# Kernel tuning notes

Hardware: AMD Instinct MI355X
Metric: run time of the kernel (lower is better)

Reference implementation:

```python
import jax, jax.numpy as jnp
import numpy as np

N_NODES = 50000


def setup_inputs() -> dict:
    key = jax.random.key(0)
    ks = jax.random.split(key, 5)
    d_in, d_out = 512, 512
    n_edges = 800000
    x = jax.random.normal(ks[0], (N_NODES, d_in), dtype=jnp.float32)
    edge_index = jax.random.randint(ks[1], (2, n_edges), 0, N_NODES, dtype=jnp.int64)
    s = 1.0 / np.sqrt(d_in)
    W_l = jax.random.uniform(ks[2], (d_out, d_in), dtype=jnp.float32, minval=-s, maxval=s)
    b_l = jax.random.uniform(ks[3], (d_out,), dtype=jnp.float32, minval=-s, maxval=s)
    W_r = jax.random.uniform(ks[4], (d_out, d_in), dtype=jnp.float32, minval=-s, maxval=s)
    return {"x": x, "edge_index": edge_index, "W_l": W_l, "b_l": b_l, "W_r": W_r}


def reference(x, edge_index, W_l, b_l, W_r):
    # lin_l: dense transform before aggregation
    x_l = x @ W_l.T + b_l                       # [N, d_out]
    src, dst = edge_index[0], edge_index[1]
    # sparse adjacency matmul (SAGE mean-neighbor aggregation):
    # out_l[i] = mean_{j in N(i)} x_l[j]
    agg = jax.ops.segment_sum(x_l[src], dst, num_segments=N_NODES)   # [N, d_out]
    deg = jax.ops.segment_sum(jnp.ones_like(src, dtype=x.dtype), dst,
                              num_segments=N_NODES)                  # [N]
    out_l = agg / jnp.maximum(deg, 1.0)[:, None]
    # lin_r: self-loop transform (no bias)
    out_r = x @ W_r.T
    return out_l + out_r
```

## Files before the change

kernel.cpp:

```cpp
#include <hip/hip_runtime.h>

typedef __bf16 bf16x8 __attribute__((ext_vector_type(8)));
typedef float floatx4 __attribute__((ext_vector_type(4)));
typedef float floatx2 __attribute__((ext_vector_type(2)));
typedef unsigned short ushortx8 __attribute__((ext_vector_type(8)));

__device__ __forceinline__ unsigned short f2b(float f) {
    union { float f; unsigned u; } v; v.f = f;
    unsigned r = v.u + 0x7fffu + ((v.u >> 16) & 1u);
    return (unsigned short)(r >> 16);
}


__global__ void deg_count_kernel(const int* __restrict__ dst, int* __restrict__ deg, int nE) {
    int e = blockIdx.x * blockDim.x + threadIdx.x;
    if (e < nE) atomicAdd(&deg[dst[e]], 1);
}

__global__ void scan1_kernel(const int* __restrict__ deg, int* __restrict__ bsum, int n) {
    __shared__ int s[256];
    int b = blockIdx.x, t = threadIdx.x;
    int base = b * 1024 + t * 4;
    int v = 0;
#pragma unroll
    for (int i = 0; i < 4; i++) { int idx = base + i; if (idx < n) v += deg[idx]; }
    s[t] = v; __syncthreads();
    for (int o = 128; o > 0; o >>= 1) { if (t < o) s[t] += s[t + o]; __syncthreads(); }
    if (t == 0) bsum[b] = s[0];
}

__global__ void scan2_kernel(int* __restrict__ bsum, int* __restrict__ off, int nb, int n) {
    if (threadIdx.x == 0) {
        int acc = 0;
        for (int i = 0; i < nb; i++) { int x = bsum[i]; bsum[i] = acc; acc += x; }
        off[n] = acc;
    }
}

__global__ void scan3_kernel(const int* __restrict__ deg, const int* __restrict__ bsum,
                             int* __restrict__ off, int n) {
    __shared__ int s[256];
    int b = blockIdx.x, t = threadIdx.x;
    int idx = b * 1024 + t * 4;
    int a0 = (idx     < n) ? deg[idx]     : 0;
    int a1 = (idx + 1 < n) ? deg[idx + 1] : 0;
    int a2 = (idx + 2 < n) ? deg[idx + 2] : 0;
    int a3 = (idx + 3 < n) ? deg[idx + 3] : 0;
    int tsum = a0 + a1 + a2 + a3;
    s[t] = tsum; __syncthreads();
    for (int o = 1; o < 256; o <<= 1) {
        int u = (t >= o) ? s[t - o] : 0;
        __syncthreads();
        s[t] += u;
        __syncthreads();
    }
    int excl = s[t] - tsum + bsum[b];
    if (idx     < n) off[idx]     = excl;
    if (idx + 1 < n) off[idx + 1] = excl + a0;
    if (idx + 2 < n) off[idx + 2] = excl + a0 + a1;
    if (idx + 3 < n) off[idx + 3] = excl + a0 + a1 + a2;
}

__global__ void fill_kernel(const int* __restrict__ src, const int* __restrict__ dst,
                            const int* __restrict__ off, int* __restrict__ cursor,
                            int* __restrict__ csr, int nE) {
    int e = blockIdx.x * blockDim.x + threadIdx.x;
    if (e < nE) {
        int d = dst[e];
        int pos = atomicAdd(&cursor[d], 1);
        csr[off[d] + pos] = src[e];
    }
}


__global__ void convx_kernel(const float* __restrict__ x, unsigned short* __restrict__ Abuf,
                             unsigned char* __restrict__ X8, int Mreal, int Mpad) {
    long t = (long)blockIdx.x * blockDim.x + threadIdx.x;
    long row = t >> 6;
    int c8 = (int)(t & 63) * 8;
    if (row >= Mpad) return;
    if (row < Mreal) {
        const float4* p4 = (const float4*)(x + row * 512 + c8);
        float4 v0 = p4[0], v1 = p4[1];
        ushortx8 o8;
        o8[0] = f2b(v0.x); o8[1] = f2b(v0.y); o8[2] = f2b(v0.z); o8[3] = f2b(v0.w);
        o8[4] = f2b(v1.x); o8[5] = f2b(v1.y); o8[6] = f2b(v1.z); o8[7] = f2b(v1.w);
        *(ushortx8*)(Abuf + row * 1024 + 512 + c8) = o8;
        unsigned int pa = __builtin_amdgcn_cvt_pk_fp8_f32(v0.x, v0.y, 0, false);
        pa = __builtin_amdgcn_cvt_pk_fp8_f32(v0.z, v0.w, pa, true);
        unsigned int pb = __builtin_amdgcn_cvt_pk_fp8_f32(v1.x, v1.y, 0, false);
        pb = __builtin_amdgcn_cvt_pk_fp8_f32(v1.z, v1.w, pb, true);
        *(uint2*)(X8 + row * 512 + c8) = make_uint2(pa, pb);
    } else {
        ushortx8 z = {0, 0, 0, 0, 0, 0, 0, 0};
        *(ushortx8*)(Abuf + row * 1024 + c8) = z;
        *(ushortx8*)(Abuf + row * 1024 + 512 + c8) = z;
    }
}


__global__ void agg_kernel(const unsigned char* __restrict__ X8,
                           const int* __restrict__ off, const int* __restrict__ csr,
                           unsigned short* __restrict__ Abuf_w, int n) {
    int wid = (int)((blockIdx.x * (long)blockDim.x + threadIdx.x) >> 6);
    int l = threadIdx.x & 63;
    if (wid >= n) return;
    int beg = off[wid], end = off[wid + 1];
    float a[8] = {};
    int e = beg;
    while (e < end) {
        int cnt = end - e; if (cnt > 64) cnt = 64;
        int myi = csr[e + (l < cnt ? l : cnt - 1)];
        for (int j = 0; j < cnt; j++) {
            int s = __builtin_amdgcn_readlane(myi, j);
            uint2 p = *(const uint2*)(X8 + (long)s * 512 + l * 8);
            floatx2 f0 = __builtin_amdgcn_cvt_pk_f32_fp8(p.x, false);
            floatx2 f1 = __builtin_amdgcn_cvt_pk_f32_fp8(p.x, true);
            floatx2 f2 = __builtin_amdgcn_cvt_pk_f32_fp8(p.y, false);
            floatx2 f3 = __builtin_amdgcn_cvt_pk_f32_fp8(p.y, true);
            a[0] += f0[0]; a[1] += f0[1]; a[2] += f1[0]; a[3] += f1[1];
            a[4] += f2[0]; a[5] += f2[1]; a[6] += f3[0]; a[7] += f3[1];
        }
        e += cnt;
    }
    int d = end - beg;
    float inv = 1.0f / (float)(d > 0 ? d : 1);
    ushortx8 o8;
#pragma unroll
    for (int i = 0; i < 8; i++) o8[i] = f2b(a[i] * inv);
    *(ushortx8*)(Abuf_w + (long)wid * 1024 + l * 8) = o8;
}


__global__ void convw_kernel(const float* __restrict__ Wl, const float* __restrict__ Wr,
                             unsigned short* __restrict__ Wcat) {
    int t = blockIdx.x * blockDim.x + threadIdx.x;
    int o = t >> 7;
    int c8 = (t & 127) * 8;
    const float* p = (c8 < 512) ? (Wl + o * 512 + c8) : (Wr + o * 512 + (c8 - 512));
    float4 v0 = ((const float4*)p)[0], v1 = ((const float4*)p)[1];
    ushortx8 o8;
    o8[0] = f2b(v0.x); o8[1] = f2b(v0.y); o8[2] = f2b(v0.z); o8[3] = f2b(v0.w);
    o8[4] = f2b(v1.x); o8[5] = f2b(v1.y); o8[6] = f2b(v1.z); o8[7] = f2b(v1.w);
    *(ushortx8*)(Wcat + (long)o * 1024 + c8) = o8;
}


__global__ __launch_bounds__(256, 2)
void gemm_kernel(const unsigned short* __restrict__ A, const unsigned short* __restrict__ B,
                 const float* __restrict__ bl, const int* __restrict__ deg,
                 float* __restrict__ out, int Mreal) {
    __shared__ unsigned short As[128 * 32];
    __shared__ unsigned short Bs[128 * 32];
    int tid = threadIdx.x;
    int w = tid >> 6, l = tid & 63;
    long i0 = (long)blockIdx.y * 128;
    int n0 = blockIdx.x * 128;
    int wm = (w >> 1) * 64, wn = (w & 1) * 64;
    int r = l & 15, q = l >> 4;
    int srow = l >> 2;
    int sch = (l & 3) * 8;

    floatx4 acc[4][4] = {};

    for (int k0 = 0; k0 < 1024; k0 += 32) {
#pragma unroll
        for (int j = 0; j < 2; j++) {
            int s = w * 2 + j;
            int row = s * 16 + srow;
            const unsigned short* ga = A + (i0 + row) * 1024 + k0 + sch;
            const unsigned short* gb = B + (long)(n0 + row) * 1024 + k0 + sch;
            __builtin_amdgcn_global_load_lds(
                (__attribute__((address_space(1))) void*)(uintptr_t)ga,
                (__attribute__((address_space(3))) void*)(uintptr_t)(As + s * 512), 16, 0, 0);
            __builtin_amdgcn_global_load_lds(
                (__attribute__((address_space(1))) void*)(uintptr_t)gb,
                (__attribute__((address_space(3))) void*)(uintptr_t)(Bs + s * 512), 16, 0, 0);
        }
        __syncthreads();
        bf16x8 af[4], bfr[4];
#pragma unroll
        for (int a = 0; a < 4; a++)
            af[a] = *(const bf16x8*)(As + (wm + a * 16 + r) * 32 + q * 8);
#pragma unroll
        for (int b = 0; b < 4; b++)
            bfr[b] = *(const bf16x8*)(Bs + (wn + b * 16 + r) * 32 + q * 8);
#pragma unroll
        for (int a = 0; a < 4; a++)
#pragma unroll
            for (int b = 0; b < 4; b++)
                acc[a][b] = __builtin_amdgcn_mfma_f32_16x16x32_bf16(af[a], bfr[b], acc[a][b], 0, 0, 0);
        __syncthreads();
    }

#pragma unroll
    for (int a = 0; a < 4; a++) {
        long rb = i0 + wm + a * 16 + q * 4;
#pragma unroll
        for (int rr = 0; rr < 4; rr++) {
            long row = rb + rr;
            if (row < Mreal) {
                bool hasdeg = deg[row] > 0;
#pragma unroll
                for (int b = 0; b < 4; b++) {
                    int col = n0 + wn + b * 16 + r;
                    float v = acc[a][b][rr];
                    if (hasdeg) v += bl[col];
                    out[row * 512 + col] = v;
                }
            }
        }
    }
}


extern "C" void kernel_launch(void* const* d_in, const int* in_sizes, int n_in,
                              void* d_out, int out_size, void* d_ws, size_t ws_size,
                              hipStream_t stream) {
    const float* x  = (const float*)d_in[0];
    const int* eidx = (const int*)d_in[1];
    const float* Wl = (const float*)d_in[2];
    const float* bl = (const float*)d_in[3];
    const float* Wr = (const float*)d_in[4];
    float* out = (float*)d_out;

    int N  = in_sizes[0] / 512;
    int nE = in_sizes[1] / 2;
    const int* src = eidx;
    const int* dst = eidx + nE;
    int Mpad = (N + 127) & ~127;
    int nb = (N + 1023) / 1024;

    char* w = (char*)d_ws;
    size_t o = 0;
    auto alloc = [&](size_t bytes) { void* p = w + o; o = (o + bytes + 255) & ~255UL; return p; };
    int* deg    = (int*)alloc((size_t)N * 4);
    int* cursor = (int*)alloc((size_t)N * 4);
    int* off    = (int*)alloc((size_t)(N + 1) * 4);
    int* bsum   = (int*)alloc((size_t)nb * 4);
    int* csr    = (int*)alloc((size_t)nE * 4);
    unsigned short* Wcat = (unsigned short*)alloc((size_t)512 * 1024 * 2);
    unsigned short* Abuf = (unsigned short*)alloc((size_t)Mpad * 1024 * 2);
    unsigned char*  X8   = (unsigned char*)alloc((size_t)Mpad * 512);
    if (o > ws_size) return;

    hipMemsetAsync(deg, 0, (size_t)N * 4, stream);
    hipMemsetAsync(cursor, 0, (size_t)N * 4, stream);

    deg_count_kernel<<<(nE + 255) / 256, 256, 0, stream>>>(dst, deg, nE);
    scan1_kernel<<<nb, 256, 0, stream>>>(deg, bsum, N);
    scan2_kernel<<<1, 64, 0, stream>>>(bsum, off, nb, N);
    scan3_kernel<<<nb, 256, 0, stream>>>(deg, bsum, off, N);
    fill_kernel<<<(nE + 255) / 256, 256, 0, stream>>>(src, dst, off, cursor, csr, nE);
    convx_kernel<<<(int)(((long)Mpad * 64 + 255) / 256), 256, 0, stream>>>(x, Abuf, X8, N, Mpad);
    convw_kernel<<<(512 * 128) / 256, 256, 0, stream>>>(Wl, Wr, Wcat);
    agg_kernel<<<(N * 64 + 255) / 256, 256, 0, stream>>>(X8, off, csr, Abuf, N);

    dim3 g(512 / 128, Mpad / 128);
    gemm_kernel<<<g, 256, 0, stream>>>(Abuf, Wcat, bl, deg, out, N);
}
```

Before: 438.9 us.

## Fuse scan stages and conversion kernels, prefetch in aggregation, swizzle GEMM grid

The single-thread middle scan is removed: each scan3 block now reduces the preceding block sums itself with a wavefront shuffle, and writes off[n] = nE directly. The x and weight conversion kernels are merged into one launch. The aggregation loop software-prefetches the next neighbor row before converting the current one. The GEMM switches to a 1D grid with a grouped tile order for L2 reuse and raises launch bounds to 3 blocks per CU. Together these aim to cut launch count and serial latency, at the cost of more register pressure in the GEMM. The in-block scan reduction only works while nb <= 64.

```diff
diff --git a/kernel.cpp b/kernel.cpp
--- a/kernel.cpp
+++ b/kernel.cpp
@@ -29,18 +29,16 @@
     if (t == 0) bsum[b] = s[0];
 }
 
-__global__ void scan2_kernel(int* __restrict__ bsum, int* __restrict__ off, int nb, int n) {
-    if (threadIdx.x == 0) {
-        int acc = 0;
-        for (int i = 0; i < nb; i++) { int x = bsum[i]; bsum[i] = acc; acc += x; }
-        off[n] = acc;
-    }
-}
-
 __global__ void scan3_kernel(const int* __restrict__ deg, const int* __restrict__ bsum,
-                             int* __restrict__ off, int n) {
+                             int* __restrict__ off, int n, int nb, int nE) {
     __shared__ int s[256];
+    __shared__ int base_s;
     int b = blockIdx.x, t = threadIdx.x;
+    if (t < 64) {
+        int v = (t < nb && t < b) ? bsum[t] : 0;
+        for (int o = 32; o > 0; o >>= 1) v += __shfl_down(v, o, 64);
+        if (t == 0) base_s = v;
+    }
     int idx = b * 1024 + t * 4;
     int a0 = (idx     < n) ? deg[idx]     : 0;
     int a1 = (idx + 1 < n) ? deg[idx + 1] : 0;
@@ -54,11 +52,12 @@
         s[t] += u;
         __syncthreads();
     }
-    int excl = s[t] - tsum + bsum[b];
+    int excl = s[t] - tsum + base_s;
     if (idx     < n) off[idx]     = excl;
     if (idx + 1 < n) off[idx + 1] = excl + a0;
     if (idx + 2 < n) off[idx + 2] = excl + a0 + a1;
     if (idx + 3 < n) off[idx + 3] = excl + a0 + a1 + a2;
+    if (b == 0 && t == 0) off[n] = nE;
 }
 
 __global__ void fill_kernel(const int* __restrict__ src, const int* __restrict__ dst,
@@ -73,28 +72,43 @@
 }
 
 
-__global__ void convx_kernel(const float* __restrict__ x, unsigned short* __restrict__ Abuf,
-                             unsigned char* __restrict__ X8, int Mreal, int Mpad) {
+__global__ void conv_kernel(const float* __restrict__ x, unsigned short* __restrict__ Abuf,
+                            unsigned char* __restrict__ X8,
+                            const float* __restrict__ Wl, const float* __restrict__ Wr,
+                            unsigned short* __restrict__ Wcat,
+                            int Mreal, long nx) {
     long t = (long)blockIdx.x * blockDim.x + threadIdx.x;
-    long row = t >> 6;
-    int c8 = (int)(t & 63) * 8;
-    if (row >= Mpad) return;
-    if (row < Mreal) {
-        const float4* p4 = (const float4*)(x + row * 512 + c8);
-        float4 v0 = p4[0], v1 = p4[1];
+    if (t < nx) {
+        long row = t >> 6;
+        int c8 = (int)(t & 63) * 8;
+        if (row < Mreal) {
+            const float4* p4 = (const float4*)(x + row * 512 + c8);
+            float4 v0 = p4[0], v1 = p4[1];
+            ushortx8 o8;
+            o8[0] = f2b(v0.x); o8[1] = f2b(v0.y); o8[2] = f2b(v0.z); o8[3] = f2b(v0.w);
+            o8[4] = f2b(v1.x); o8[5] = f2b(v1.y); o8[6] = f2b(v1.z); o8[7] = f2b(v1.w);
+            *(ushortx8*)(Abuf + row * 1024 + 512 + c8) = o8;
+            unsigned int pa = __builtin_amdgcn_cvt_pk_fp8_f32(v0.x, v0.y, 0, false);
+            pa = __builtin_amdgcn_cvt_pk_fp8_f32(v0.z, v0.w, pa, true);
+            unsigned int pb = __builtin_amdgcn_cvt_pk_fp8_f32(v1.x, v1.y, 0, false);
+            pb = __builtin_amdgcn_cvt_pk_fp8_f32(v1.z, v1.w, pb, true);
+            *(uint2*)(X8 + row * 512 + c8) = make_uint2(pa, pb);
+        } else {
+            ushortx8 z = {0, 0, 0, 0, 0, 0, 0, 0};
+            *(ushortx8*)(Abuf + row * 1024 + c8) = z;
+            *(ushortx8*)(Abuf + row * 1024 + 512 + c8) = z;
+        }
+    } else {
+        long u = t - nx;
+        if (u >= 65536) return;
+        int o = (int)(u >> 7);
+        int c8 = (int)(u & 127) * 8;
+        const float* p = (c8 < 512) ? (Wl + o * 512 + c8) : (Wr + o * 512 + (c8 - 512));
+        float4 v0 = ((const float4*)p)[0], v1 = ((const float4*)p)[1];
         ushortx8 o8;
         o8[0] = f2b(v0.x); o8[1] = f2b(v0.y); o8[2] = f2b(v0.z); o8[3] = f2b(v0.w);
         o8[4] = f2b(v1.x); o8[5] = f2b(v1.y); o8[6] = f2b(v1.z); o8[7] = f2b(v1.w);
-        *(ushortx8*)(Abuf + row * 1024 + 512 + c8) = o8;
-        unsigned int pa = __builtin_amdgcn_cvt_pk_fp8_f32(v0.x, v0.y, 0, false);
-        pa = __builtin_amdgcn_cvt_pk_fp8_f32(v0.z, v0.w, pa, true);
-        unsigned int pb = __builtin_amdgcn_cvt_pk_fp8_f32(v1.x, v1.y, 0, false);
-        pb = __builtin_amdgcn_cvt_pk_fp8_f32(v1.z, v1.w, pb, true);
-        *(uint2*)(X8 + row * 512 + c8) = make_uint2(pa, pb);
-    } else {
-        ushortx8 z = {0, 0, 0, 0, 0, 0, 0, 0};
-        *(ushortx8*)(Abuf + row * 1024 + c8) = z;
-        *(ushortx8*)(Abuf + row * 1024 + 512 + c8) = z;
+        *(ushortx8*)(Wcat + (long)o * 1024 + c8) = o8;
     }
 }
 
@@ -111,15 +125,26 @@
     while (e < end) {
         int cnt = end - e; if (cnt > 64) cnt = 64;
         int myi = csr[e + (l < cnt ? l : cnt - 1)];
-        for (int j = 0; j < cnt; j++) {
+        int s0 = __builtin_amdgcn_readlane(myi, 0);
+        uint2 p = *(const uint2*)(X8 + (long)s0 * 512 + l * 8);
+        for (int j = 1; j < cnt; j++) {
             int s = __builtin_amdgcn_readlane(myi, j);
-            uint2 p = *(const uint2*)(X8 + (long)s * 512 + l * 8);
+            uint2 pn = *(const uint2*)(X8 + (long)s * 512 + l * 8);
             floatx2 f0 = __builtin_amdgcn_cvt_pk_f32_fp8(p.x, false);
             floatx2 f1 = __builtin_amdgcn_cvt_pk_f32_fp8(p.x, true);
             floatx2 f2 = __builtin_amdgcn_cvt_pk_f32_fp8(p.y, false);
             floatx2 f3 = __builtin_amdgcn_cvt_pk_f32_fp8(p.y, true);
             a[0] += f0[0]; a[1] += f0[1]; a[2] += f1[0]; a[3] += f1[1];
             a[4] += f2[0]; a[5] += f2[1]; a[6] += f3[0]; a[7] += f3[1];
+            p = pn;
+        }
+        {
+            floatx2 f0 = __builtin_amdgcn_cvt_pk_f32_fp8(p.x, false);
+            floatx2 f1 = __builtin_amdgcn_cvt_pk_f32_fp8(p.x, true);
+            floatx2 f2 = __builtin_amdgcn_cvt_pk_f32_fp8(p.y, false);
+            floatx2 f3 = __builtin_amdgcn_cvt_pk_f32_fp8(p.y, true);
+            a[0] += f0[0]; a[1] += f0[1]; a[2] += f1[0]; a[3] += f1[1];
+            a[4] += f2[0]; a[5] += f2[1]; a[6] += f3[0]; a[7] += f3[1];
         }
         e += cnt;
     }
@@ -132,30 +157,21 @@
 }
 
 
-__global__ void convw_kernel(const float* __restrict__ Wl, const float* __restrict__ Wr,
-                             unsigned short* __restrict__ Wcat) {
-    int t = blockIdx.x * blockDim.x + threadIdx.x;
-    int o = t >> 7;
-    int c8 = (t & 127) * 8;
-    const float* p = (c8 < 512) ? (Wl + o * 512 + c8) : (Wr + o * 512 + (c8 - 512));
-    float4 v0 = ((const float4*)p)[0], v1 = ((const float4*)p)[1];
-    ushortx8 o8;
-    o8[0] = f2b(v0.x); o8[1] = f2b(v0.y); o8[2] = f2b(v0.z); o8[3] = f2b(v0.w);
-    o8[4] = f2b(v1.x); o8[5] = f2b(v1.y); o8[6] = f2b(v1.z); o8[7] = f2b(v1.w);
-    *(ushortx8*)(Wcat + (long)o * 1024 + c8) = o8;
-}
-
-
-__global__ __launch_bounds__(256, 2)
+__global__ __launch_bounds__(256, 3)
 void gemm_kernel(const unsigned short* __restrict__ A, const unsigned short* __restrict__ B,
                  const float* __restrict__ bl, const int* __restrict__ deg,
-                 float* __restrict__ out, int Mreal) {
+                 float* __restrict__ out, int Mreal, int nby) {
+    int L = blockIdx.x;
+    int by = (L >> 5) * 8 + (L & 7);
+    int bx = (L >> 3) & 3;
+    if (by >= nby) return;
+
     __shared__ unsigned short As[128 * 32];
     __shared__ unsigned short Bs[128 * 32];
     int tid = threadIdx.x;
     int w = tid >> 6, l = tid & 63;
-    long i0 = (long)blockIdx.y * 128;
-    int n0 = blockIdx.x * 128;
+    long i0 = (long)by * 128;
+    int n0 = bx * 128;
     int wm = (w >> 1) * 64, wn = (w & 1) * 64;
     int r = l & 15, q = l >> 4;
     int srow = l >> 2;
@@ -230,6 +246,7 @@
     const int* dst = eidx + nE;
     int Mpad = (N + 127) & ~127;
     int nb = (N + 1023) / 1024;
+    int nby = Mpad / 128;
 
     char* w = (char*)d_ws;
     size_t o = 0;
@@ -249,13 +266,12 @@
 
     deg_count_kernel<<<(nE + 255) / 256, 256, 0, stream>>>(dst, deg, nE);
     scan1_kernel<<<nb, 256, 0, stream>>>(deg, bsum, N);
-    scan2_kernel<<<1, 64, 0, stream>>>(bsum, off, nb, N);
-    scan3_kernel<<<nb, 256, 0, stream>>>(deg, bsum, off, N);
+    scan3_kernel<<<nb, 256, 0, stream>>>(deg, bsum, off, N, nb, nE);
     fill_kernel<<<(nE + 255) / 256, 256, 0, stream>>>(src, dst, off, cursor, csr, nE);
-    convx_kernel<<<(int)(((long)Mpad * 64 + 255) / 256), 256, 0, stream>>>(x, Abuf, X8, N, Mpad);
-    convw_kernel<<<(512 * 128) / 256, 256, 0, stream>>>(Wl, Wr, Wcat);
+    long nx = (long)Mpad * 64;
+    conv_kernel<<<(int)((nx + 65536 + 255) / 256), 256, 0, stream>>>(x, Abuf, X8, Wl, Wr, Wcat, N, nx);
     agg_kernel<<<(N * 64 + 255) / 256, 256, 0, stream>>>(X8, off, csr, Abuf, N);
 
-    dim3 g(512 / 128, Mpad / 128);
-    gemm_kernel<<<g, 256, 0, stream>>>(Abuf, Wcat, bl, deg, out, N);
-}
+    int nbyp = (nby + 7) & ~7;
+    gemm_kernel<<<nbyp * 4, 256, 0, stream>>>(Abuf, Wcat, bl, deg, out, N, nby);
+}
```

After: 412.2 us. 6.1% less time.
